# Kernel tuning notes

Hardware: AMD Instinct MI355X
Metric: run time of the kernel (lower is better)

The kernel has to match this reference:

```python
import jax, jax.numpy as jnp
import numpy as np

PF_DIM = 1024
F_DIM = 1024
LOW = 128
MID = 32  # low_dim // 4
BATCH = 8192


def setup_inputs() -> dict:
    key = jax.random.key(0)
    ks = jax.random.split(key, 10)
    s = lambda fan_in: 1.0 / np.sqrt(fan_in)
    return {
        "f": jax.random.normal(ks[0], (BATCH, F_DIM), jnp.float32),
        "pf": jax.random.normal(ks[1], (BATCH, PF_DIM), jnp.float32),
        # nn.Linear weights are (out, in)
        "proj_f_w": jax.random.uniform(ks[2], (LOW, F_DIM), jnp.float32, -s(F_DIM), s(F_DIM)),
        "proj_f_b": jax.random.uniform(ks[3], (LOW,), jnp.float32, -s(F_DIM), s(F_DIM)),
        "proj_pf_w": jax.random.uniform(ks[4], (LOW, PF_DIM), jnp.float32, -s(PF_DIM), s(PF_DIM)),
        "proj_pf_b": jax.random.uniform(ks[5], (LOW,), jnp.float32, -s(PF_DIM), s(PF_DIM)),
        "proj_f2_w": jax.random.uniform(ks[6], (F_DIM, LOW), jnp.float32, -s(LOW), s(LOW)),
        "proj_f2_b": jax.random.uniform(ks[7], (F_DIM,), jnp.float32, -s(LOW), s(LOW)),
        "pg_w": jax.random.uniform(ks[8], (2 * LOW * MID, LOW), jnp.float32, -s(LOW), s(LOW)),
        "pg_b": jax.random.uniform(ks[9], (2 * LOW * MID,), jnp.float32, -s(LOW), s(LOW)),
    }


def reference(f, pf, proj_f_w, proj_f_b, proj_pf_w, proj_pf_b,
              proj_f2_w, proj_f2_b, pg_w, pg_b):
    b = pf.shape[0]
    # project both inputs to low_dim
    f_low = f @ proj_f_w.T + proj_f_b              # (b, LOW)
    pf_low = pf @ proj_pf_w.T + proj_pf_b          # (b, LOW)
    # per-sample generated weights
    params = pf_low @ pg_w.T + pg_b                # (b, 2*LOW*MID)
    dim = LOW * MID
    p1 = params[:, :dim].reshape(b, LOW, MID)      # (b, LOW, MID)
    p2 = params[:, dim:].reshape(b, MID, LOW)      # (b, MID, LOW)
    # batched tiny MLP: (b,1,LOW)@(b,LOW,MID) -> relu -> @(b,MID,LOW)
    h = jax.nn.relu(jnp.einsum('bl,blm->bm', f_low, p1))
    g = jnp.einsum('bm,bml->bl', h, p2)            # (b, LOW)
    out = g @ proj_f2_w.T + proj_f2_b + f + pf     # (b, F_DIM)
    return out
```

## Files before the change

### kernel.cpp

```cpp
#include <hip/hip_runtime.h>
#include <stdint.h>


typedef __attribute__((ext_vector_type(8))) short bf16x8;
typedef __attribute__((ext_vector_type(4))) float f32x4;

#define MFMA(a, b, c) __builtin_amdgcn_mfma_f32_16x16x32_bf16((a), (b), (c), 0, 0, 0)

__device__ __forceinline__ ushort f2bf(float x) {
    union { float f; uint32_t u; } v; v.f = x;
    return (ushort)((v.u + 0x7FFFu + ((v.u >> 16) & 1u)) >> 16);
}
__device__ __forceinline__ ushort4 f2bf4(float4 v) {
    ushort4 o; o.x = f2bf(v.x); o.y = f2bf(v.y); o.z = f2bf(v.z); o.w = f2bf(v.w); return o;
}
__device__ __forceinline__ float bf2f(ushort u) {
    union { uint32_t i; float f; } v; v.i = ((uint32_t)u) << 16; return v.f;
}

__global__ __launch_bounds__(256) void k0_convert(
    const float* __restrict__ pgw, const float* __restrict__ wf,
    const float* __restrict__ wpf, const float* __restrict__ w2,
    ushort* __restrict__ pg_img, ushort* __restrict__ w_img, ushort* __restrict__ w2_img)
{
    int cid = blockIdx.x * 256 + threadIdx.x;
    const float* src; ushort* dst;
    if (cid < 131072) {
        int lane = cid & 63, ks = (cid >> 6) & 3, T = cid >> 8;
        int j = T * 16 + (lane & 15), k = ks * 32 + (lane >> 4) * 8;
        src = pgw + (size_t)j * 128 + k;
        dst = pg_img + (size_t)cid * 8;
    } else if (cid < 163840) {
        int c = cid - 131072;
        int lane = c & 63, ks = (c >> 6) & 31, lt = (c >> 11) & 7, mat = c >> 14;
        int l = lt * 16 + (lane & 15), k = ks * 32 + (lane >> 4) * 8;
        src = (mat ? wpf : wf) + (size_t)l * 1024 + k;
        dst = w_img + (size_t)c * 8;
    } else {
        int c = cid - 163840;
        int lane = c & 63, ks = (c >> 6) & 3, nt = c >> 8;
        int n = nt * 16 + (lane & 15), k = ks * 32 + (lane >> 4) * 8;
        src = w2 + (size_t)n * 128 + k;
        dst = w2_img + (size_t)c * 8;
    }
    float4 a = ((const float4*)src)[0], b = ((const float4*)src)[1];
    ((ushort4*)dst)[0] = f2bf4(a);
    ((ushort4*)dst)[1] = f2bf4(b);
}

__global__ __launch_bounds__(512, 2) void mega(
    const float* __restrict__ f, const float* __restrict__ pf,
    const ushort* __restrict__ w_img, const float* __restrict__ bfb,
    const float* __restrict__ bpfb, const ushort* __restrict__ pg_img,
    const float* __restrict__ pgb, const ushort* __restrict__ w2_img,
    const float* __restrict__ b2, float* __restrict__ out)
{
    __shared__ __align__(16) char smem[62464];
    ushort* As    = (ushort*)smem;
    ushort* Tr    = (ushort*)smem;
    float*  hred  = (float*)smem;
    float*  hl    = (float*)(smem + 32768);
    float*  gred  = (float*)smem;
    float*  Ls    = (float*)smem;
    ushort* flowT = (ushort*)(smem + 36864);
    ushort* pfrag = (ushort*)(smem + 46080);
    ushort* gfrag = (ushort*)(smem + 54272);

    const int tid = threadIdx.x;
    const int lane = tid & 63, wid = tid >> 6;
    const int q = lane >> 4, r15 = lane & 15;
    const int b0 = blockIdx.x * 32;

#pragma unroll 1
    for (int mat = 0; mat < 2; mat++) {
        const float* src = mat ? pf : f;
        const float* bias_ptr = mat ? bpfb : bfb;
        float bias_v = bias_ptr[wid * 16 + r15];

        f32x4 c[2];
        c[0] = (f32x4){0.f, 0.f, 0.f, 0.f};
        c[1] = (f32x4){0.f, 0.f, 0.f, 0.f};

#pragma unroll 1
        for (int kh = 0; kh < 2; kh++) {
            __syncthreads();
            float4 v[8];
#pragma unroll
            for (int rr = 0; rr < 8; rr++) {
                int row = rr * 4 + (tid >> 7);
                v[rr] = *(const float4*)(src + (size_t)(b0 + row) * 1024 + kh * 512 + (tid & 127) * 4);
            }
#pragma unroll
            for (int rr = 0; rr < 8; rr++) {
                int row = rr * 4 + (tid >> 7);
                *(ushort4*)(As + row * 520 + (tid & 127) * 4) = f2bf4(v[rr]);
            }
            __syncthreads();
            const ushort* wb = w_img + (size_t)mat * 131072 + ((size_t)wid * 32 + kh * 16) * 512;
            bf16x8 wfr[4];
#pragma unroll
            for (int p = 0; p < 4; p++) wfr[p] = *(const bf16x8*)(wb + (size_t)p * 512 + lane * 8);
#pragma unroll
            for (int ks = 0; ks < 16; ks++) {
                const int cur = ks & 3;
                bf16x8 a0 = *(const bf16x8*)(As + (size_t)r15 * 520 + ks * 32 + q * 8);
                bf16x8 a1 = *(const bf16x8*)(As + (size_t)(16 + r15) * 520 + ks * 32 + q * 8);
                c[0] = MFMA(a0, wfr[cur], c[0]);
                c[1] = MFMA(a1, wfr[cur], c[1]);
                if (ks + 4 < 16)
                    wfr[cur] = *(const bf16x8*)(wb + (size_t)(ks + 4) * 512 + lane * 8);
            }
        }
        if (mat == 0) {
#pragma unroll
            for (int mt = 0; mt < 2; mt++) {
                int l = wid * 16 + r15;
#pragma unroll
                for (int r = 0; r < 4; r++)
                    flowT[l * 36 + mt * 16 + q * 4 + r] = f2bf(c[mt][r] + bias_v);
            }
        } else {
            __syncthreads();
#pragma unroll
            for (int mt = 0; mt < 2; mt++) {
                int l = wid * 16 + r15;
#pragma unroll
                for (int r = 0; r < 4; r++)
                    Tr[(mt * 16 + q * 4 + r) * 136 + l] = f2bf(c[mt][r] + bias_v);
            }
            __syncthreads();
            {
                int bt = wid >> 2, ks2 = wid & 3;
                int k0 = ks2 * 32 + (lane >> 4) * 8;
                uint4 tv = *(const uint4*)(Tr + (size_t)(bt * 16 + (lane & 15)) * 136 + k0);
                *(uint4*)(pfrag + (size_t)wid * 512 + lane * 8) = tv;
            }
        }
    }
    __syncthreads();

    bf16x8 bfr[2][4];
#pragma unroll
    for (int ct = 0; ct < 2; ct++)
#pragma unroll
        for (int ks = 0; ks < 4; ks++)
            bfr[ct][ks] = *(const bf16x8*)(pfrag + (size_t)(ct * 4 + ks) * 512 + lane * 8);

    f32x4 hacc[2][2];
    hacc[0][0] = hacc[0][1] = hacc[1][0] = hacc[1][1] = (f32x4){0.f, 0.f, 0.f, 0.f};

#pragma unroll 1
    for (int jg = 0; jg < 8; jg++) {
        const ushort* Tbase = pg_img + (size_t)(jg * 32 + wid * 4) * 2048;
        bf16x8 af[4][4];
#pragma unroll
        for (int i = 0; i < 4; i++)
#pragma unroll
            for (int ks = 0; ks < 4; ks++)
                af[i][ks] = *(const bf16x8*)(Tbase + (size_t)i * 2048 + ks * 512 + lane * 8);
#pragma unroll
        for (int i = 0; i < 4; i++) {
            const int tl = wid * 4 + i;
            const int mh = i & 1;
            const int l_loc = tl >> 1;
            f32x4 bv = *(const f32x4*)(pgb + (size_t)(jg * 32 + tl) * 16 + q * 4);
            const int fbase = (jg * 16 + l_loc) * 36;
#pragma unroll
            for (int ct = 0; ct < 2; ct++) {
                f32x4 cc = (f32x4){0.f, 0.f, 0.f, 0.f};
#pragma unroll
                for (int ks = 0; ks < 4; ks++) cc = MFMA(af[i][ks], bfr[ct][ks], cc);
                float s = bf2f(flowT[fbase + ct * 16 + r15]);
#pragma unroll
                for (int r = 0; r < 4; r++) hacc[mh][ct][r] += s * (cc[r] + bv[r]);
            }
        }
    }
#pragma unroll
    for (int mh = 0; mh < 2; mh++)
#pragma unroll
        for (int ct = 0; ct < 2; ct++)
#pragma unroll
            for (int r = 0; r < 4; r++)
                hred[wid * 1024 + (mh * 16 + q * 4 + r) * 32 + ct * 16 + r15] = hacc[mh][ct][r];
    __syncthreads();
    {
        int m = tid >> 4, bc = (tid & 15) * 2;
        float s0 = 0.f, s1 = 0.f;
#pragma unroll
        for (int w = 0; w < 8; w++) {
            s0 += hred[w * 1024 + m * 32 + bc];
            s1 += hred[w * 1024 + m * 32 + bc + 1];
        }
        hl[m * 32 + bc]     = fmaxf(s0, 0.f);
        hl[m * 32 + bc + 1] = fmaxf(s1, 0.f);
    }
    __syncthreads();

#pragma unroll 1
    for (int lg = 0; lg < 4; lg++) {
        f32x4 gacc[2][2];
        gacc[0][0] = gacc[0][1] = gacc[1][0] = gacc[1][1] = (f32x4){0.f, 0.f, 0.f, 0.f};
        bf16x8 af[4][4];
#pragma unroll
        for (int t = 0; t < 4; t++) {
            const int m = wid + 8 * (t >> 1), lt = t & 1;
            const ushort* ap = pg_img + (size_t)(256 + m * 8 + lg * 2 + lt) * 2048;
#pragma unroll
            for (int ks = 0; ks < 4; ks++)
                af[t][ks] = *(const bf16x8*)(ap + ks * 512 + lane * 8);
        }
#pragma unroll
        for (int ti = 0; ti < 8; ti++) {
            const int cur = ti & 3;
            const int m = wid + 8 * (ti >> 1), lt = ti & 1;
            f32x4 bv = *(const f32x4*)(pgb + 4096 + (size_t)m * 128 + lg * 32 + lt * 16 + q * 4);
#pragma unroll
            for (int ct = 0; ct < 2; ct++) {
                f32x4 cc = (f32x4){0.f, 0.f, 0.f, 0.f};
#pragma unroll
                for (int ks = 0; ks < 4; ks++) cc = MFMA(af[cur][ks], bfr[ct][ks], cc);
                float s = hl[m * 32 + ct * 16 + r15];
#pragma unroll
                for (int r = 0; r < 4; r++) gacc[lt][ct][r] += s * (cc[r] + bv[r]);
            }
            if (ti + 4 < 8) {
                const int tn = ti + 4;
                const int mn = wid + 8 * (tn >> 1), ltn = tn & 1;
                const ushort* ap = pg_img + (size_t)(256 + mn * 8 + lg * 2 + ltn) * 2048;
#pragma unroll
                for (int ks = 0; ks < 4; ks++)
                    af[cur][ks] = *(const bf16x8*)(ap + ks * 512 + lane * 8);
            }
        }
#pragma unroll
        for (int lt = 0; lt < 2; lt++)
#pragma unroll
            for (int ct = 0; ct < 2; ct++)
#pragma unroll
                for (int r = 0; r < 4; r++)
                    gred[wid * 1024 + (lt * 16 + q * 4 + r) * 32 + ct * 16 + r15] = gacc[lt][ct][r];
        __syncthreads();
        if (tid < 128) {
            int bt = tid >> 6, ln = tid & 63;
            int b_loc = bt * 16 + (ln & 15);
            int l0 = (ln >> 4) * 8;
            ushort tmp[8];
#pragma unroll
            for (int e = 0; e < 8; e++) {
                const float* gp = gred + (size_t)(l0 + e) * 32 + b_loc;
                float s = 0.f;
#pragma unroll
                for (int w = 0; w < 8; w++) s += gp[w * 1024];
                tmp[e] = f2bf(s);
            }
            ushort4 lo = {tmp[0], tmp[1], tmp[2], tmp[3]};
            ushort4 hi = {tmp[4], tmp[5], tmp[6], tmp[7]};
            ushort* dst = gfrag + (size_t)(bt * 4 + lg) * 512 + ln * 8;
            ((ushort4*)dst)[0] = lo;
            ((ushort4*)dst)[1] = hi;
        }
        __syncthreads();
    }

    bf16x8 afg[2][4];
#pragma unroll
    for (int mtl = 0; mtl < 2; mtl++)
#pragma unroll
        for (int ks = 0; ks < 4; ks++)
            afg[mtl][ks] = *(const bf16x8*)(gfrag + (size_t)(mtl * 4 + ks) * 512 + lane * 8);

#pragma unroll 1
    for (int nb = 0; nb < 4; nb++) {
        float bias_v2[2];
#pragma unroll
        for (int nt = 0; nt < 2; nt++) bias_v2[nt] = b2[nb * 256 + wid * 32 + nt * 16 + r15];
        bf16x8 wfr2[2][4];
#pragma unroll
        for (int nt = 0; nt < 2; nt++)
#pragma unroll
            for (int ks = 0; ks < 4; ks++)
                wfr2[nt][ks] = *(const bf16x8*)(w2_img + (size_t)((nb * 16 + wid * 2 + nt) * 4 + ks) * 512 + lane * 8);
#pragma unroll
        for (int nt = 0; nt < 2; nt++) {
#pragma unroll
            for (int mtl = 0; mtl < 2; mtl++) {
                f32x4 cc = (f32x4){0.f, 0.f, 0.f, 0.f};
#pragma unroll
                for (int ks = 0; ks < 4; ks++) cc = MFMA(afg[mtl][ks], wfr2[nt][ks], cc);
#pragma unroll
                for (int r = 0; r < 4; r++)
                    Ls[(size_t)(mtl * 16 + q * 4 + r) * 288 + wid * 36 + nt * 16 + r15] = cc[r] + bias_v2[nt];
            }
        }
        __syncthreads();
        {
            const float* ls = Ls + (size_t)(wid * 4) * 288 + (lane >> 3) * 36 + (lane & 7) * 4;
            const int n0 = nb * 256;
#pragma unroll
            for (int rr = 0; rr < 4; rr++) {
                const int b = b0 + wid * 4 + rr;
                const size_t gbase = (size_t)b * 1024 + n0 + lane * 4;
                float4 lv = *(const float4*)(ls + rr * 288);
                float4 fa = *(const float4*)(f + gbase);
                float4 pa = *(const float4*)(pf + gbase);
                float4 o;
                o.x = lv.x + fa.x + pa.x; o.y = lv.y + fa.y + pa.y;
                o.z = lv.z + fa.z + pa.z; o.w = lv.w + fa.w + pa.w;
                *(float4*)(out + gbase) = o;
            }
        }
        __syncthreads();
    }
}

extern "C" void kernel_launch(void* const* d_in, const int* in_sizes, int n_in,
                              void* d_out, int out_size, void* d_ws, size_t ws_size,
                              hipStream_t stream)
{
    const float* f    = (const float*)d_in[0];
    const float* pf   = (const float*)d_in[1];
    const float* wf   = (const float*)d_in[2];
    const float* bfb  = (const float*)d_in[3];
    const float* wpf  = (const float*)d_in[4];
    const float* bpfb = (const float*)d_in[5];
    const float* w2   = (const float*)d_in[6];
    const float* b2   = (const float*)d_in[7];
    const float* pgw  = (const float*)d_in[8];
    const float* pgb  = (const float*)d_in[9];

    char* ws = (char*)d_ws;
    ushort* pg_img = (ushort*)(ws + 0);
    ushort* w_img  = (ushort*)(ws + 2097152);
    ushort* w2_img = (ushort*)(ws + 2621440);
    float*  out    = (float*)d_out;

    k0_convert<<<dim3(704), dim3(256), 0, stream>>>(pgw, wf, wpf, w2, pg_img, w_img, w2_img);
    mega<<<dim3(256), dim3(512), 0, stream>>>(f, pf, w_img, bfb, bpfb,
                                              pg_img, pgb, w2_img, b2, out);
}
```

Baseline: 180.9 us.

## Double block size to 16 waves and split per-wave work across them

The fused kernel now launches 1024 threads per block instead of 512 and redistributes work across the 16 waves. Each wave handles half of the former tiles: one M-tile in the projection GEMMs, one sample column tile in the generated-weight stages, and one N-tile in the final projection. This raises per-block wave parallelism for latency hiding on the 256-block grid, which otherwise underfills the CUs. The cost is that each pg_img weight fragment is now loaded by two waves instead of one, and the launch bound tightens the register budget.

```diff
diff --git a/kernel.cpp b/kernel.cpp
--- a/kernel.cpp
+++ b/kernel.cpp
@@ -48,7 +48,7 @@
     ((ushort4*)dst)[1] = f2bf4(b);
 }
 
-__global__ __launch_bounds__(512, 2) void mega(
+__global__ __launch_bounds__(1024, 4) void mega(
     const float* __restrict__ f, const float* __restrict__ pf,
     const ushort* __restrict__ w_img, const float* __restrict__ bfb,
     const float* __restrict__ bpfb, const ushort* __restrict__ pg_img,
@@ -69,89 +69,82 @@
     const int tid = threadIdx.x;
     const int lane = tid & 63, wid = tid >> 6;
     const int q = lane >> 4, r15 = lane & 15;
+    const int pw = wid & 7, ctw = wid >> 3;
     const int b0 = blockIdx.x * 32;
 
-#pragma unroll 1
-    for (int mat = 0; mat < 2; mat++) {
-        const float* src = mat ? pf : f;
-        const float* bias_ptr = mat ? bpfb : bfb;
-        float bias_v = bias_ptr[wid * 16 + r15];
-
-        f32x4 c[2];
-        c[0] = (f32x4){0.f, 0.f, 0.f, 0.f};
-        c[1] = (f32x4){0.f, 0.f, 0.f, 0.f};
-
-#pragma unroll 1
-        for (int kh = 0; kh < 2; kh++) {
-            __syncthreads();
-            float4 v[8];
-#pragma unroll
-            for (int rr = 0; rr < 8; rr++) {
-                int row = rr * 4 + (tid >> 7);
-                v[rr] = *(const float4*)(src + (size_t)(b0 + row) * 1024 + kh * 512 + (tid & 127) * 4);
-            }
-#pragma unroll
-            for (int rr = 0; rr < 8; rr++) {
-                int row = rr * 4 + (tid >> 7);
-                *(ushort4*)(As + row * 520 + (tid & 127) * 4) = f2bf4(v[rr]);
-            }
-            __syncthreads();
-            const ushort* wb = w_img + (size_t)mat * 131072 + ((size_t)wid * 32 + kh * 16) * 512;
-            bf16x8 wfr[4];
-#pragma unroll
-            for (int p = 0; p < 4; p++) wfr[p] = *(const bf16x8*)(wb + (size_t)p * 512 + lane * 8);
-#pragma unroll
-            for (int ks = 0; ks < 16; ks++) {
-                const int cur = ks & 3;
-                bf16x8 a0 = *(const bf16x8*)(As + (size_t)r15 * 520 + ks * 32 + q * 8);
-                bf16x8 a1 = *(const bf16x8*)(As + (size_t)(16 + r15) * 520 + ks * 32 + q * 8);
-                c[0] = MFMA(a0, wfr[cur], c[0]);
-                c[1] = MFMA(a1, wfr[cur], c[1]);
-                if (ks + 4 < 16)
-                    wfr[cur] = *(const bf16x8*)(wb + (size_t)(ks + 4) * 512 + lane * 8);
-            }
-        }
-        if (mat == 0) {
-#pragma unroll
-            for (int mt = 0; mt < 2; mt++) {
-                int l = wid * 16 + r15;
+    {
+        const int lt = wid >> 1, mt = wid & 1;
+#pragma unroll 1
+        for (int mat = 0; mat < 2; mat++) {
+            const float* src = mat ? pf : f;
+            const float* bias_ptr = mat ? bpfb : bfb;
+            float bias_v = bias_ptr[lt * 16 + r15];
+
+            f32x4 c = (f32x4){0.f, 0.f, 0.f, 0.f};
+
+#pragma unroll 1
+            for (int kh = 0; kh < 2; kh++) {
+                __syncthreads();
+                float4 v[4];
+#pragma unroll
+                for (int rr = 0; rr < 4; rr++) {
+                    int row = rr * 8 + (tid >> 7);
+                    v[rr] = *(const float4*)(src + (size_t)(b0 + row) * 1024 + kh * 512 + (tid & 127) * 4);
+                }
+#pragma unroll
+                for (int rr = 0; rr < 4; rr++) {
+                    int row = rr * 8 + (tid >> 7);
+                    *(ushort4*)(As + row * 520 + (tid & 127) * 4) = f2bf4(v[rr]);
+                }
+                __syncthreads();
+                const ushort* wb = w_img + (size_t)mat * 131072 + ((size_t)lt * 32 + kh * 16) * 512;
+                bf16x8 wfr[4];
+#pragma unroll
+                for (int p = 0; p < 4; p++) wfr[p] = *(const bf16x8*)(wb + (size_t)p * 512 + lane * 8);
+#pragma unroll
+                for (int ks = 0; ks < 16; ks++) {
+                    const int cur = ks & 3;
+                    bf16x8 a0 = *(const bf16x8*)(As + (size_t)(mt * 16 + r15) * 520 + ks * 32 + q * 8);
+                    c = MFMA(a0, wfr[cur], c);
+                    if (ks + 4 < 16)
+                        wfr[cur] = *(const bf16x8*)(wb + (size_t)(ks + 4) * 512 + lane * 8);
+                }
+            }
+            if (mat == 0) {
+                int l = lt * 16 + r15;
 #pragma unroll
                 for (int r = 0; r < 4; r++)
-                    flowT[l * 36 + mt * 16 + q * 4 + r] = f2bf(c[mt][r] + bias_v);
-            }
-        } else {
-            __syncthreads();
-#pragma unroll
-            for (int mt = 0; mt < 2; mt++) {
-                int l = wid * 16 + r15;
+                    flowT[l * 36 + mt * 16 + q * 4 + r] = f2bf(c[r] + bias_v);
+            } else {
+                __syncthreads();
+                int l = lt * 16 + r15;
 #pragma unroll
                 for (int r = 0; r < 4; r++)
-                    Tr[(mt * 16 + q * 4 + r) * 136 + l] = f2bf(c[mt][r] + bias_v);
-            }
-            __syncthreads();
-            {
-                int bt = wid >> 2, ks2 = wid & 3;
-                int k0 = ks2 * 32 + (lane >> 4) * 8;
-                uint4 tv = *(const uint4*)(Tr + (size_t)(bt * 16 + (lane & 15)) * 136 + k0);
-                *(uint4*)(pfrag + (size_t)wid * 512 + lane * 8) = tv;
+                    Tr[(mt * 16 + q * 4 + r) * 136 + l] = f2bf(c[r] + bias_v);
+                __syncthreads();
+                if (wid < 8) {
+                    int bt = wid >> 2, ks2 = wid & 3;
+                    int k0 = ks2 * 32 + (lane >> 4) * 8;
+                    uint4 tv = *(const uint4*)(Tr + (size_t)(bt * 16 + (lane & 15)) * 136 + k0);
+                    *(uint4*)(pfrag + (size_t)wid * 512 + lane * 8) = tv;
+                }
             }
         }
     }
     __syncthreads();
 
-    bf16x8 bfr[2][4];
-#pragma unroll
-    for (int ct = 0; ct < 2; ct++)
-#pragma unroll
-        for (int ks = 0; ks < 4; ks++)
-            bfr[ct][ks] = *(const bf16x8*)(pfrag + (size_t)(ct * 4 + ks) * 512 + lane * 8);
-
-    f32x4 hacc[2][2];
-    hacc[0][0] = hacc[0][1] = hacc[1][0] = hacc[1][1] = (f32x4){0.f, 0.f, 0.f, 0.f};
+    bf16x8 bfr[4];
+#pragma unroll
+    for (int ks = 0; ks < 4; ks++)
+        bfr[ks] = *(const bf16x8*)(pfrag + (size_t)(ctw * 4 + ks) * 512 + lane * 8);
+
+    f32x4 hacc[2];
+    hacc[0] = (f32x4){0.f, 0.f, 0.f, 0.f};
+    hacc[1] = (f32x4){0.f, 0.f, 0.f, 0.f};
 
 #pragma unroll 1
     for (int jg = 0; jg < 8; jg++) {
-        const ushort* Tbase = pg_img + (size_t)(jg * 32 + wid * 4) * 2048;
+        const ushort* Tbase = pg_img + (size_t)(jg * 32 + pw * 4) * 2048;
         bf16x8 af[4][4];
 #pragma unroll
         for (int i = 0; i < 4; i++)
@@ -160,51 +153,42 @@
                 af[i][ks] = *(const bf16x8*)(Tbase + (size_t)i * 2048 + ks * 512 + lane * 8);
 #pragma unroll
         for (int i = 0; i < 4; i++) {
-            const int tl = wid * 4 + i;
+            const int tl = pw * 4 + i;
             const int mh = i & 1;
             const int l_loc = tl >> 1;
             f32x4 bv = *(const f32x4*)(pgb + (size_t)(jg * 32 + tl) * 16 + q * 4);
-            const int fbase = (jg * 16 + l_loc) * 36;
-#pragma unroll
-            for (int ct = 0; ct < 2; ct++) {
-                f32x4 cc = (f32x4){0.f, 0.f, 0.f, 0.f};
-#pragma unroll
-                for (int ks = 0; ks < 4; ks++) cc = MFMA(af[i][ks], bfr[ct][ks], cc);
-                float s = bf2f(flowT[fbase + ct * 16 + r15]);
-#pragma unroll
-                for (int r = 0; r < 4; r++) hacc[mh][ct][r] += s * (cc[r] + bv[r]);
-            }
+            f32x4 cc = (f32x4){0.f, 0.f, 0.f, 0.f};
+#pragma unroll
+            for (int ks = 0; ks < 4; ks++) cc = MFMA(af[i][ks], bfr[ks], cc);
+            float s = bf2f(flowT[(jg * 16 + l_loc) * 36 + ctw * 16 + r15]);
+#pragma unroll
+            for (int r = 0; r < 4; r++) hacc[mh][r] += s * (cc[r] + bv[r]);
         }
     }
 #pragma unroll
     for (int mh = 0; mh < 2; mh++)
 #pragma unroll
-        for (int ct = 0; ct < 2; ct++)
-#pragma unroll
-            for (int r = 0; r < 4; r++)
-                hred[wid * 1024 + (mh * 16 + q * 4 + r) * 32 + ct * 16 + r15] = hacc[mh][ct][r];
+        for (int r = 0; r < 4; r++)
+            hred[pw * 1024 + (mh * 16 + q * 4 + r) * 32 + ctw * 16 + r15] = hacc[mh][r];
     __syncthreads();
     {
-        int m = tid >> 4, bc = (tid & 15) * 2;
-        float s0 = 0.f, s1 = 0.f;
-#pragma unroll
-        for (int w = 0; w < 8; w++) {
-            s0 += hred[w * 1024 + m * 32 + bc];
-            s1 += hred[w * 1024 + m * 32 + bc + 1];
-        }
-        hl[m * 32 + bc]     = fmaxf(s0, 0.f);
-        hl[m * 32 + bc + 1] = fmaxf(s1, 0.f);
+        int m = tid >> 5, bc = tid & 31;
+        float s = 0.f;
+#pragma unroll
+        for (int w = 0; w < 8; w++) s += hred[w * 1024 + m * 32 + bc];
+        hl[m * 32 + bc] = fmaxf(s, 0.f);
     }
     __syncthreads();
 
 #pragma unroll 1
     for (int lg = 0; lg < 4; lg++) {
-        f32x4 gacc[2][2];
-        gacc[0][0] = gacc[0][1] = gacc[1][0] = gacc[1][1] = (f32x4){0.f, 0.f, 0.f, 0.f};
+        f32x4 gacc[2];
+        gacc[0] = (f32x4){0.f, 0.f, 0.f, 0.f};
+        gacc[1] = (f32x4){0.f, 0.f, 0.f, 0.f};
         bf16x8 af[4][4];
 #pragma unroll
         for (int t = 0; t < 4; t++) {
-            const int m = wid + 8 * (t >> 1), lt = t & 1;
+            const int m = pw + 8 * (t >> 1), lt = t & 1;
             const ushort* ap = pg_img + (size_t)(256 + m * 8 + lg * 2 + lt) * 2048;
 #pragma unroll
             for (int ks = 0; ks < 4; ks++)
@@ -213,20 +197,17 @@
 #pragma unroll
         for (int ti = 0; ti < 8; ti++) {
             const int cur = ti & 3;
-            const int m = wid + 8 * (ti >> 1), lt = ti & 1;
+            const int m = pw + 8 * (ti >> 1), lt = ti & 1;
             f32x4 bv = *(const f32x4*)(pgb + 4096 + (size_t)m * 128 + lg * 32 + lt * 16 + q * 4);
-#pragma unroll
-            for (int ct = 0; ct < 2; ct++) {
-                f32x4 cc = (f32x4){0.f, 0.f, 0.f, 0.f};
-#pragma unroll
-                for (int ks = 0; ks < 4; ks++) cc = MFMA(af[cur][ks], bfr[ct][ks], cc);
-                float s = hl[m * 32 + ct * 16 + r15];
-#pragma unroll
-                for (int r = 0; r < 4; r++) gacc[lt][ct][r] += s * (cc[r] + bv[r]);
-            }
+            f32x4 cc = (f32x4){0.f, 0.f, 0.f, 0.f};
+#pragma unroll
+            for (int ks = 0; ks < 4; ks++) cc = MFMA(af[cur][ks], bfr[ks], cc);
+            float s = hl[m * 32 + ctw * 16 + r15];
+#pragma unroll
+            for (int r = 0; r < 4; r++) gacc[lt][r] += s * (cc[r] + bv[r]);
             if (ti + 4 < 8) {
                 const int tn = ti + 4;
-                const int mn = wid + 8 * (tn >> 1), ltn = tn & 1;
+                const int mn = pw + 8 * (tn >> 1), ltn = tn & 1;
                 const ushort* ap = pg_img + (size_t)(256 + mn * 8 + lg * 2 + ltn) * 2048;
 #pragma unroll
                 for (int ks = 0; ks < 4; ks++)
@@ -236,10 +217,8 @@
 #pragma unroll
         for (int lt = 0; lt < 2; lt++)
 #pragma unroll
-            for (int ct = 0; ct < 2; ct++)
-#pragma unroll
-                for (int r = 0; r < 4; r++)
-                    gred[wid * 1024 + (lt * 16 + q * 4 + r) * 32 + ct * 16 + r15] = gacc[lt][ct][r];
+            for (int r = 0; r < 4; r++)
+                gred[pw * 1024 + (lt * 16 + q * 4 + r) * 32 + ctw * 16 + r15] = gacc[lt][r];
         __syncthreads();
         if (tid < 128) {
             int bt = tid >> 6, ln = tid & 63;
@@ -272,34 +251,27 @@
 
 #pragma unroll 1
     for (int nb = 0; nb < 4; nb++) {
-        float bias_v2[2];
-#pragma unroll
-        for (int nt = 0; nt < 2; nt++) bias_v2[nt] = b2[nb * 256 + wid * 32 + nt * 16 + r15];
-        bf16x8 wfr2[2][4];
-#pragma unroll
-        for (int nt = 0; nt < 2; nt++)
-#pragma unroll
-            for (int ks = 0; ks < 4; ks++)
-                wfr2[nt][ks] = *(const bf16x8*)(w2_img + (size_t)((nb * 16 + wid * 2 + nt) * 4 + ks) * 512 + lane * 8);
-#pragma unroll
-        for (int nt = 0; nt < 2; nt++) {
-#pragma unroll
-            for (int mtl = 0; mtl < 2; mtl++) {
-                f32x4 cc = (f32x4){0.f, 0.f, 0.f, 0.f};
-#pragma unroll
-                for (int ks = 0; ks < 4; ks++) cc = MFMA(afg[mtl][ks], wfr2[nt][ks], cc);
-#pragma unroll
-                for (int r = 0; r < 4; r++)
-                    Ls[(size_t)(mtl * 16 + q * 4 + r) * 288 + wid * 36 + nt * 16 + r15] = cc[r] + bias_v2[nt];
-            }
+        float bias_v = b2[nb * 256 + wid * 16 + r15];
+        bf16x8 wfr2[4];
+#pragma unroll
+        for (int ks = 0; ks < 4; ks++)
+            wfr2[ks] = *(const bf16x8*)(w2_img + (size_t)((nb * 16 + wid) * 4 + ks) * 512 + lane * 8);
+#pragma unroll
+        for (int mtl = 0; mtl < 2; mtl++) {
+            f32x4 cc = (f32x4){0.f, 0.f, 0.f, 0.f};
+#pragma unroll
+            for (int ks = 0; ks < 4; ks++) cc = MFMA(afg[mtl][ks], wfr2[ks], cc);
+#pragma unroll
+            for (int r = 0; r < 4; r++)
+                Ls[(size_t)(mtl * 16 + q * 4 + r) * 288 + (wid >> 1) * 36 + (wid & 1) * 16 + r15] = cc[r] + bias_v;
         }
         __syncthreads();
         {
-            const float* ls = Ls + (size_t)(wid * 4) * 288 + (lane >> 3) * 36 + (lane & 7) * 4;
+            const float* ls = Ls + (size_t)(wid * 2) * 288 + (lane >> 3) * 36 + (lane & 7) * 4;
             const int n0 = nb * 256;
 #pragma unroll
-            for (int rr = 0; rr < 4; rr++) {
-                const int b = b0 + wid * 4 + rr;
+            for (int rr = 0; rr < 2; rr++) {
+                const int b = b0 + wid * 2 + rr;
                 const size_t gbase = (size_t)b * 1024 + n0 + lane * 4;
                 float4 lv = *(const float4*)(ls + rr * 288);
                 float4 fa = *(const float4*)(f + gbase);
@@ -336,6 +308,6 @@
     float*  out    = (float*)d_out;
 
     k0_convert<<<dim3(704), dim3(256), 0, stream>>>(pgw, wf, wpf, w2, pg_img, w_img, w2_img);
-    mega<<<dim3(256), dim3(512), 0, stream>>>(f, pf, w_img, bfb, bpfb,
-                                              pg_img, pgb, w2_img, b2, out);
-}
+    mega<<<dim3(256), dim3(1024), 0, stream>>>(f, pf, w_img, bfb, bpfb,
+                                               pg_img, pgb, w2_img, b2, out);
+}
```

After: 210.6 us. +16.4%, slower.

## Software-pipeline global loads across all stages of the fused kernel

Applied to the files above, without the earlier changes.

Prefetches the next input tile (f/pf chunk) into registers while the current one is converted and multiplied. It also fully unrolls the generated-weight loops with a rolling 4-deep register prefetch of pg_img fragments and biases across iteration-group boundaries. In the final projection it double-buffers the w2 fragments and issues the residual f/pf loads before the MFMA work. The aim is to hide global-memory latency behind compute, at the cost of higher register pressure and larger unrolled code.

```diff
diff --git a/kernel.cpp b/kernel.cpp
--- a/kernel.cpp
+++ b/kernel.cpp
@@ -71,31 +71,39 @@
     const int q = lane >> 4, r15 = lane & 15;
     const int b0 = blockIdx.x * 32;
 
-#pragma unroll 1
-    for (int mat = 0; mat < 2; mat++) {
-        const float* src = mat ? pf : f;
-        const float* bias_ptr = mat ? bpfb : bfb;
-        float bias_v = bias_ptr[wid * 16 + r15];
-
+    {
+        float4 vbuf[8];
+#pragma unroll
+        for (int rr = 0; rr < 8; rr++) {
+            int row = rr * 4 + (tid >> 7);
+            vbuf[rr] = *(const float4*)(f + (size_t)(b0 + row) * 1024 + (tid & 127) * 4);
+        }
         f32x4 c[2];
-        c[0] = (f32x4){0.f, 0.f, 0.f, 0.f};
-        c[1] = (f32x4){0.f, 0.f, 0.f, 0.f};
-
-#pragma unroll 1
-        for (int kh = 0; kh < 2; kh++) {
-            __syncthreads();
-            float4 v[8];
+        float bias_v = 0.f;
+#pragma unroll
+        for (int s = 0; s < 4; s++) {
+            const int mat = s >> 1, kh = s & 1;
+            if (kh == 0) {
+                c[0] = (f32x4){0.f, 0.f, 0.f, 0.f};
+                c[1] = (f32x4){0.f, 0.f, 0.f, 0.f};
+                bias_v = (mat ? bpfb : bfb)[wid * 16 + r15];
+            }
+            __syncthreads();
 #pragma unroll
             for (int rr = 0; rr < 8; rr++) {
                 int row = rr * 4 + (tid >> 7);
-                v[rr] = *(const float4*)(src + (size_t)(b0 + row) * 1024 + kh * 512 + (tid & 127) * 4);
-            }
-#pragma unroll
-            for (int rr = 0; rr < 8; rr++) {
-                int row = rr * 4 + (tid >> 7);
-                *(ushort4*)(As + row * 520 + (tid & 127) * 4) = f2bf4(v[rr]);
-            }
-            __syncthreads();
+                *(ushort4*)(As + row * 520 + (tid & 127) * 4) = f2bf4(vbuf[rr]);
+            }
+            __syncthreads();
+            if (s < 3) {
+                const int sn = s + 1, matn = sn >> 1, khn = sn & 1;
+                const float* srcn = matn ? pf : f;
+#pragma unroll
+                for (int rr = 0; rr < 8; rr++) {
+                    int row = rr * 4 + (tid >> 7);
+                    vbuf[rr] = *(const float4*)(srcn + (size_t)(b0 + row) * 1024 + khn * 512 + (tid & 127) * 4);
+                }
+            }
             const ushort* wb = w_img + (size_t)mat * 131072 + ((size_t)wid * 32 + kh * 16) * 512;
             bf16x8 wfr[4];
 #pragma unroll
@@ -110,26 +118,23 @@
                 if (ks + 4 < 16)
                     wfr[cur] = *(const bf16x8*)(wb + (size_t)(ks + 4) * 512 + lane * 8);
             }
-        }
-        if (mat == 0) {
-#pragma unroll
-            for (int mt = 0; mt < 2; mt++) {
+            if (s == 1) {
                 int l = wid * 16 + r15;
 #pragma unroll
-                for (int r = 0; r < 4; r++)
-                    flowT[l * 36 + mt * 16 + q * 4 + r] = f2bf(c[mt][r] + bias_v);
-            }
-        } else {
-            __syncthreads();
-#pragma unroll
-            for (int mt = 0; mt < 2; mt++) {
+                for (int mt = 0; mt < 2; mt++)
+#pragma unroll
+                    for (int r = 0; r < 4; r++)
+                        flowT[l * 36 + mt * 16 + q * 4 + r] = f2bf(c[mt][r] + bias_v);
+            }
+            if (s == 3) {
+                __syncthreads();
                 int l = wid * 16 + r15;
 #pragma unroll
-                for (int r = 0; r < 4; r++)
-                    Tr[(mt * 16 + q * 4 + r) * 136 + l] = f2bf(c[mt][r] + bias_v);
-            }
-            __syncthreads();
-            {
+                for (int mt = 0; mt < 2; mt++)
+#pragma unroll
+                    for (int r = 0; r < 4; r++)
+                        Tr[(mt * 16 + q * 4 + r) * 136 + l] = f2bf(c[mt][r] + bias_v);
+                __syncthreads();
                 int bt = wid >> 2, ks2 = wid & 3;
                 int k0 = ks2 * 32 + (lane >> 4) * 8;
                 uint4 tv = *(const uint4*)(Tr + (size_t)(bt * 16 + (lane & 15)) * 136 + k0);
@@ -149,30 +154,45 @@
     f32x4 hacc[2][2];
     hacc[0][0] = hacc[0][1] = hacc[1][0] = hacc[1][1] = (f32x4){0.f, 0.f, 0.f, 0.f};
 
-#pragma unroll 1
-    for (int jg = 0; jg < 8; jg++) {
-        const ushort* Tbase = pg_img + (size_t)(jg * 32 + wid * 4) * 2048;
+    {
         bf16x8 af[4][4];
-#pragma unroll
-        for (int i = 0; i < 4; i++)
+        f32x4 bvr[4];
+#pragma unroll
+        for (int t = 0; t < 4; t++) {
+            const int tl = wid * 4 + t;
+            const ushort* ap = pg_img + (size_t)tl * 2048;
 #pragma unroll
             for (int ks = 0; ks < 4; ks++)
-                af[i][ks] = *(const bf16x8*)(Tbase + (size_t)i * 2048 + ks * 512 + lane * 8);
-#pragma unroll
-        for (int i = 0; i < 4; i++) {
-            const int tl = wid * 4 + i;
-            const int mh = i & 1;
-            const int l_loc = tl >> 1;
-            f32x4 bv = *(const f32x4*)(pgb + (size_t)(jg * 32 + tl) * 16 + q * 4);
-            const int fbase = (jg * 16 + l_loc) * 36;
-#pragma unroll
-            for (int ct = 0; ct < 2; ct++) {
-                f32x4 cc = (f32x4){0.f, 0.f, 0.f, 0.f};
-#pragma unroll
-                for (int ks = 0; ks < 4; ks++) cc = MFMA(af[i][ks], bfr[ct][ks], cc);
-                float s = bf2f(flowT[fbase + ct * 16 + r15]);
-#pragma unroll
-                for (int r = 0; r < 4; r++) hacc[mh][ct][r] += s * (cc[r] + bv[r]);
+                af[t][ks] = *(const bf16x8*)(ap + ks * 512 + lane * 8);
+            bvr[t] = *(const f32x4*)(pgb + (size_t)tl * 16 + q * 4);
+        }
+#pragma unroll
+        for (int jg = 0; jg < 8; jg++) {
+#pragma unroll
+            for (int i = 0; i < 4; i++) {
+                const int t = jg * 4 + i, cur = t & 3;
+                const int tl = wid * 4 + i;
+                const int mh = i & 1;
+                const int l_loc = tl >> 1;
+                f32x4 bv = bvr[cur];
+#pragma unroll
+                for (int ct = 0; ct < 2; ct++) {
+                    f32x4 cc = (f32x4){0.f, 0.f, 0.f, 0.f};
+#pragma unroll
+                    for (int ks = 0; ks < 4; ks++) cc = MFMA(af[cur][ks], bfr[ct][ks], cc);
+                    float s = bf2f(flowT[(jg * 16 + l_loc) * 36 + ct * 16 + r15]);
+#pragma unroll
+                    for (int r = 0; r < 4; r++) hacc[mh][ct][r] += s * (cc[r] + bv[r]);
+                }
+                if (t + 4 < 32) {
+                    const int tn = t + 4, jgn = tn >> 2, in = tn & 3;
+                    const int tln = jgn * 32 + wid * 4 + in;
+                    const ushort* ap = pg_img + (size_t)tln * 2048;
+#pragma unroll
+                    for (int ks = 0; ks < 4; ks++)
+                        af[cur][ks] = *(const bf16x8*)(ap + ks * 512 + lane * 8);
+                    bvr[cur] = *(const f32x4*)(pgb + (size_t)tln * 16 + q * 4);
+                }
             }
         }
     }
@@ -197,120 +217,144 @@
     }
     __syncthreads();
 
-#pragma unroll 1
-    for (int lg = 0; lg < 4; lg++) {
-        f32x4 gacc[2][2];
-        gacc[0][0] = gacc[0][1] = gacc[1][0] = gacc[1][1] = (f32x4){0.f, 0.f, 0.f, 0.f};
-        bf16x8 af[4][4];
+    {
+        bf16x8 afc[4][4];
+        f32x4 bvc[4];
 #pragma unroll
         for (int t = 0; t < 4; t++) {
             const int m = wid + 8 * (t >> 1), lt = t & 1;
-            const ushort* ap = pg_img + (size_t)(256 + m * 8 + lg * 2 + lt) * 2048;
+            const ushort* ap = pg_img + (size_t)(256 + m * 8 + lt) * 2048;
 #pragma unroll
             for (int ks = 0; ks < 4; ks++)
-                af[t][ks] = *(const bf16x8*)(ap + ks * 512 + lane * 8);
-        }
-#pragma unroll
-        for (int ti = 0; ti < 8; ti++) {
-            const int cur = ti & 3;
-            const int m = wid + 8 * (ti >> 1), lt = ti & 1;
-            f32x4 bv = *(const f32x4*)(pgb + 4096 + (size_t)m * 128 + lg * 32 + lt * 16 + q * 4);
-#pragma unroll
-            for (int ct = 0; ct < 2; ct++) {
-                f32x4 cc = (f32x4){0.f, 0.f, 0.f, 0.f};
-#pragma unroll
-                for (int ks = 0; ks < 4; ks++) cc = MFMA(af[cur][ks], bfr[ct][ks], cc);
-                float s = hl[m * 32 + ct * 16 + r15];
-#pragma unroll
-                for (int r = 0; r < 4; r++) gacc[lt][ct][r] += s * (cc[r] + bv[r]);
-            }
-            if (ti + 4 < 8) {
-                const int tn = ti + 4;
-                const int mn = wid + 8 * (tn >> 1), ltn = tn & 1;
-                const ushort* ap = pg_img + (size_t)(256 + mn * 8 + lg * 2 + ltn) * 2048;
-#pragma unroll
-                for (int ks = 0; ks < 4; ks++)
-                    af[cur][ks] = *(const bf16x8*)(ap + ks * 512 + lane * 8);
-            }
-        }
-#pragma unroll
-        for (int lt = 0; lt < 2; lt++)
-#pragma unroll
-            for (int ct = 0; ct < 2; ct++)
-#pragma unroll
-                for (int r = 0; r < 4; r++)
-                    gred[wid * 1024 + (lt * 16 + q * 4 + r) * 32 + ct * 16 + r15] = gacc[lt][ct][r];
-        __syncthreads();
-        if (tid < 128) {
-            int bt = tid >> 6, ln = tid & 63;
-            int b_loc = bt * 16 + (ln & 15);
-            int l0 = (ln >> 4) * 8;
-            ushort tmp[8];
-#pragma unroll
-            for (int e = 0; e < 8; e++) {
-                const float* gp = gred + (size_t)(l0 + e) * 32 + b_loc;
-                float s = 0.f;
-#pragma unroll
-                for (int w = 0; w < 8; w++) s += gp[w * 1024];
-                tmp[e] = f2bf(s);
-            }
-            ushort4 lo = {tmp[0], tmp[1], tmp[2], tmp[3]};
-            ushort4 hi = {tmp[4], tmp[5], tmp[6], tmp[7]};
-            ushort* dst = gfrag + (size_t)(bt * 4 + lg) * 512 + ln * 8;
-            ((ushort4*)dst)[0] = lo;
-            ((ushort4*)dst)[1] = hi;
-        }
-        __syncthreads();
-    }
-
-    bf16x8 afg[2][4];
-#pragma unroll
-    for (int mtl = 0; mtl < 2; mtl++)
-#pragma unroll
-        for (int ks = 0; ks < 4; ks++)
-            afg[mtl][ks] = *(const bf16x8*)(gfrag + (size_t)(mtl * 4 + ks) * 512 + lane * 8);
-
-#pragma unroll 1
-    for (int nb = 0; nb < 4; nb++) {
-        float bias_v2[2];
-#pragma unroll
-        for (int nt = 0; nt < 2; nt++) bias_v2[nt] = b2[nb * 256 + wid * 32 + nt * 16 + r15];
-        bf16x8 wfr2[2][4];
+                afc[t][ks] = *(const bf16x8*)(ap + ks * 512 + lane * 8);
+            bvc[t] = *(const f32x4*)(pgb + 4096 + (size_t)m * 128 + lt * 16 + q * 4);
+        }
+#pragma unroll
+        for (int lg = 0; lg < 4; lg++) {
+            f32x4 gacc[2][2];
+            gacc[0][0] = gacc[0][1] = gacc[1][0] = gacc[1][1] = (f32x4){0.f, 0.f, 0.f, 0.f};
+#pragma unroll
+            for (int ti = 0; ti < 8; ti++) {
+                const int t = lg * 8 + ti, cur = t & 3;
+                const int m = wid + 8 * (ti >> 1), lt = ti & 1;
+                f32x4 bv = bvc[cur];
+#pragma unroll
+                for (int ct = 0; ct < 2; ct++) {
+                    f32x4 cc = (f32x4){0.f, 0.f, 0.f, 0.f};
+#pragma unroll
+                    for (int ks = 0; ks < 4; ks++) cc = MFMA(afc[cur][ks], bfr[ct][ks], cc);
+                    float s = hl[m * 32 + ct * 16 + r15];
+#pragma unroll
+                    for (int r = 0; r < 4; r++) gacc[lt][ct][r] += s * (cc[r] + bv[r]);
+                }
+                if (t + 4 < 32) {
+                    const int tn = t + 4, lgn = tn >> 3, tin = tn & 7;
+                    const int mn = wid + 8 * (tin >> 1), ltn = tin & 1;
+                    const ushort* ap = pg_img + (size_t)(256 + mn * 8 + lgn * 2 + ltn) * 2048;
+#pragma unroll
+                    for (int ks = 0; ks < 4; ks++)
+                        afc[cur][ks] = *(const bf16x8*)(ap + ks * 512 + lane * 8);
+                    bvc[cur] = *(const f32x4*)(pgb + 4096 + (size_t)mn * 128 + lgn * 32 + ltn * 16 + q * 4);
+                }
+            }
+#pragma unroll
+            for (int lt = 0; lt < 2; lt++)
+#pragma unroll
+                for (int ct = 0; ct < 2; ct++)
+#pragma unroll
+                    for (int r = 0; r < 4; r++)
+                        gred[wid * 1024 + (lt * 16 + q * 4 + r) * 32 + ct * 16 + r15] = gacc[lt][ct][r];
+            __syncthreads();
+            if (tid < 128) {
+                int bt = tid >> 6, ln = tid & 63;
+                int b_loc = bt * 16 + (ln & 15);
+                int l0 = (ln >> 4) * 8;
+                ushort tmp[8];
+#pragma unroll
+                for (int e = 0; e < 8; e++) {
+                    const float* gp = gred + (size_t)(l0 + e) * 32 + b_loc;
+                    float s = 0.f;
+#pragma unroll
+                    for (int w = 0; w < 8; w++) s += gp[w * 1024];
+                    tmp[e] = f2bf(s);
+                }
+                ushort4 lo = {tmp[0], tmp[1], tmp[2], tmp[3]};
+                ushort4 hi = {tmp[4], tmp[5], tmp[6], tmp[7]};
+                ushort* dst = gfrag + (size_t)(bt * 4 + lg) * 512 + ln * 8;
+                ((ushort4*)dst)[0] = lo;
+                ((ushort4*)dst)[1] = hi;
+            }
+            __syncthreads();
+        }
+    }
+
+    {
+        bf16x8 afg[2][4];
+#pragma unroll
+        for (int mtl = 0; mtl < 2; mtl++)
+#pragma unroll
+            for (int ks = 0; ks < 4; ks++)
+                afg[mtl][ks] = *(const bf16x8*)(gfrag + (size_t)(mtl * 4 + ks) * 512 + lane * 8);
+
+        bf16x8 w2r[2][2][4];
 #pragma unroll
         for (int nt = 0; nt < 2; nt++)
 #pragma unroll
             for (int ks = 0; ks < 4; ks++)
-                wfr2[nt][ks] = *(const bf16x8*)(w2_img + (size_t)((nb * 16 + wid * 2 + nt) * 4 + ks) * 512 + lane * 8);
-#pragma unroll
-        for (int nt = 0; nt < 2; nt++) {
-#pragma unroll
-            for (int mtl = 0; mtl < 2; mtl++) {
-                f32x4 cc = (f32x4){0.f, 0.f, 0.f, 0.f};
-#pragma unroll
-                for (int ks = 0; ks < 4; ks++) cc = MFMA(afg[mtl][ks], wfr2[nt][ks], cc);
-#pragma unroll
-                for (int r = 0; r < 4; r++)
-                    Ls[(size_t)(mtl * 16 + q * 4 + r) * 288 + wid * 36 + nt * 16 + r15] = cc[r] + bias_v2[nt];
-            }
-        }
-        __syncthreads();
-        {
-            const float* ls = Ls + (size_t)(wid * 4) * 288 + (lane >> 3) * 36 + (lane & 7) * 4;
+                w2r[0][nt][ks] = *(const bf16x8*)(w2_img + (size_t)((wid * 2 + nt) * 4 + ks) * 512 + lane * 8);
+
+#pragma unroll
+        for (int nb = 0; nb < 4; nb++) {
+            const int cur = nb & 1;
             const int n0 = nb * 256;
+            float4 fa[4], pa[4];
 #pragma unroll
             for (int rr = 0; rr < 4; rr++) {
                 const int b = b0 + wid * 4 + rr;
                 const size_t gbase = (size_t)b * 1024 + n0 + lane * 4;
-                float4 lv = *(const float4*)(ls + rr * 288);
-                float4 fa = *(const float4*)(f + gbase);
-                float4 pa = *(const float4*)(pf + gbase);
-                float4 o;
-                o.x = lv.x + fa.x + pa.x; o.y = lv.y + fa.y + pa.y;
-                o.z = lv.z + fa.z + pa.z; o.w = lv.w + fa.w + pa.w;
-                *(float4*)(out + gbase) = o;
-            }
-        }
-        __syncthreads();
+                fa[rr] = *(const float4*)(f + gbase);
+                pa[rr] = *(const float4*)(pf + gbase);
+            }
+            float bias_v2[2];
+#pragma unroll
+            for (int nt = 0; nt < 2; nt++) bias_v2[nt] = b2[nb * 256 + wid * 32 + nt * 16 + r15];
+#pragma unroll
+            for (int nt = 0; nt < 2; nt++) {
+#pragma unroll
+                for (int mtl = 0; mtl < 2; mtl++) {
+                    f32x4 cc = (f32x4){0.f, 0.f, 0.f, 0.f};
+#pragma unroll
+                    for (int ks = 0; ks < 4; ks++) cc = MFMA(afg[mtl][ks], w2r[cur][nt][ks], cc);
+                    const int nloc = wid * 32 + nt * 16 + r15;
+                    const int chunk = nloc >> 5, within = nloc & 31;
+#pragma unroll
+                    for (int r = 0; r < 4; r++)
+                        Ls[(size_t)(mtl * 16 + q * 4 + r) * 288 + chunk * 36 + within] = cc[r] + bias_v2[nt];
+                }
+            }
+            if (nb < 3) {
+#pragma unroll
+                for (int nt = 0; nt < 2; nt++)
+#pragma unroll
+                    for (int ks = 0; ks < 4; ks++)
+                        w2r[cur ^ 1][nt][ks] = *(const bf16x8*)(w2_img + (size_t)(((nb + 1) * 16 + wid * 2 + nt) * 4 + ks) * 512 + lane * 8);
+            }
+            __syncthreads();
+            {
+                const float* ls = Ls + (size_t)(wid * 4) * 288 + (lane >> 3) * 36 + (lane & 7) * 4;
+#pragma unroll
+                for (int rr = 0; rr < 4; rr++) {
+                    const int b = b0 + wid * 4 + rr;
+                    const size_t gbase = (size_t)b * 1024 + n0 + lane * 4;
+                    float4 lv = *(const float4*)(ls + rr * 288);
+                    float4 o;
+                    o.x = lv.x + fa[rr].x + pa[rr].x; o.y = lv.y + fa[rr].y + pa[rr].y;
+                    o.z = lv.z + fa[rr].z + pa[rr].z; o.w = lv.w + fa[rr].w + pa[rr].w;
+                    *(float4*)(out + gbase) = o;
+                }
+            }
+            __syncthreads();
+        }
     }
 }
 
```

Result: faster. 176.5 us (-2.4%).
